# Optimization experiments

Measured on AMD Instinct MI355X. Metric: run time of the kernel, lower is better.

## Reference

```python
import jax, jax.numpy as jnp
import numpy as np

N = 100000      # nodes
E = 1600000     # edges (avg degree 16)
DIN = 128       # input_dim
H = 64          # hidden_dim -> intermediate width 2*H = 128
BN_EPS = 1e-5


def setup_inputs() -> dict:
    key = jax.random.key(0)
    ks = jax.random.split(key, 6)
    x = jax.random.normal(ks[0], (N, DIN), dtype=jnp.float32)
    edge_index = jax.random.randint(ks[1], (2, E), 0, N, dtype=jnp.int64)
    W1 = jax.random.normal(ks[2], (DIN, 2 * H), dtype=jnp.float32) / np.sqrt(DIN).astype(np.float32)
    b1 = jnp.zeros((2 * H,), jnp.float32)
    W2 = jax.random.normal(ks[3], (2 * H, H), dtype=jnp.float32) / np.sqrt(2 * H).astype(np.float32)
    b2 = jnp.zeros((H,), jnp.float32)
    gamma = jnp.ones((2 * H,), jnp.float32)
    beta = jnp.zeros((2 * H,), jnp.float32)
    prelu_a = jnp.asarray(0.25, jnp.float32)  # PReLU default single weight
    return {"x": x, "edge_index": edge_index, "W1": W1, "b1": b1,
            "W2": W2, "b2": b2, "gamma": gamma, "beta": beta, "prelu_a": prelu_a}


def _gcn_conv(x, W, b, src, dst, n):
    # PyG GCNConv (edge_weight=None): lin -> add self-loops -> sym-norm aggregate -> +bias
    h = x @ W                                             # [N, F]
    loops = jnp.arange(n, dtype=src.dtype)
    s = jnp.concatenate([src, loops])                     # [E+N]
    d = jnp.concatenate([dst, loops])
    deg = jax.ops.segment_sum(jnp.ones_like(s, jnp.float32), d, num_segments=n)
    dinv = jnp.where(deg > 0, jax.lax.rsqrt(deg), 0.0)    # deg^{-1/2}, 0 for isolated
    norm = dinv[s] * dinv[d]                              # [E+N]
    out = jax.ops.segment_sum(h[s] * norm[:, None], d, num_segments=n)
    return out + b


def reference(x, edge_index, W1, b1, W2, b2, gamma, beta, prelu_a):
    src, dst = edge_index[0], edge_index[1]
    z = _gcn_conv(x, W1, b1, src, dst, N)                 # conv1: [N, 2H]
    mean = jnp.mean(z, axis=0)                            # BatchNorm1d (training stats)
    var = jnp.var(z, axis=0)
    z = (z - mean) * (gamma * jax.lax.rsqrt(var + BN_EPS)) + beta
    z = jnp.where(z >= 0, z, prelu_a * z)                 # PReLU
    z = _gcn_conv(z, W2, b2, src, dst, N)                 # conv2: [N, H]
    return z
```

## Files before the change

### kernel.cpp

```cpp
#include <hip/hip_runtime.h>


#define DIN 128
#define F1  128
#define F2  64
#define BN_EPS 1e-5f
#define NODE_BSHIFT 8
#define NODE_BMASK  255
#define CHUNK 8192

typedef __attribute__((ext_vector_type(8))) short bf16x8;
typedef __attribute__((ext_vector_type(4))) float f32x4;
typedef __attribute__((ext_vector_type(2))) float f32x2;

__device__ __forceinline__ unsigned short f2bf(float f) {
    unsigned int u = __float_as_uint(f);
    u = u + 0x7fffu + ((u >> 16) & 1u);
    return (unsigned short)(u >> 16);
}
__device__ __forceinline__ float bf2f(unsigned short u) { return __uint_as_float((unsigned int)u << 16); }
__device__ __forceinline__ float bf_lo(unsigned int v) { return __uint_as_float(v << 16); }
__device__ __forceinline__ float bf_hi(unsigned int v) { return __uint_as_float(v & 0xffff0000u); }


__global__ __launch_bounds__(256) void hist_k(const int* __restrict__ dst,
                                              int* __restrict__ bucketcnt,
                                              int e, int nbuck) {
    __shared__ int lh[512];
    int t = threadIdx.x;
    for (int i = t; i < 512; i += 256) lh[i] = 0;
    __syncthreads();
    int base = blockIdx.x * CHUNK;
    int end = base + CHUNK; if (end > e) end = e;
    for (int i = base + t; i < end; i += 256)
        atomicAdd(&lh[dst[i] >> NODE_BSHIFT], 1);
    __syncthreads();
    for (int b = t; b < nbuck; b += 256) {
        int v = lh[b];
        if (v) atomicAdd(&bucketcnt[b], v);
    }
}

__global__ __launch_bounds__(512) void bscan_k(const int* __restrict__ bucketcnt,
                                               int* __restrict__ bucketbase,
                                               int* __restrict__ bucketcur,
                                               int* __restrict__ rowptr,
                                               int nbuck, int n, int e) {
    __shared__ int s[512];
    int t = threadIdx.x;
    int orig = (t < nbuck) ? bucketcnt[t] : 0;
    s[t] = orig;
    __syncthreads();
    int run = orig;
    for (int ofs = 1; ofs < 512; ofs <<= 1) {
        int y = (t >= ofs) ? s[t - ofs] : 0;
        __syncthreads();
        run += y;
        s[t] = run;
        __syncthreads();
    }
    if (t < nbuck) {
        int excl = run - orig;
        bucketbase[t] = excl;
        bucketcur[t] = excl;
    }
    if (t == 0) {
        bucketbase[nbuck] = e;
        rowptr[n] = e;
    }
}

__global__ __launch_bounds__(256) void binpass_k(const int* __restrict__ src,
                                                 const int* __restrict__ dst,
                                                 int* __restrict__ bucketcur,
                                                 int2* __restrict__ pairs, int e) {
    __shared__ int lh[512], lbase[512], lrank[512];
    int t = threadIdx.x;
    for (int i = t; i < 512; i += 256) { lh[i] = 0; lrank[i] = 0; }
    __syncthreads();
    int base = blockIdx.x * CHUNK;
    int end = base + CHUNK; if (end > e) end = e;
    for (int i = base + t; i < end; i += 256)
        atomicAdd(&lh[dst[i] >> NODE_BSHIFT], 1);
    __syncthreads();
    for (int b = t; b < 512; b += 256) {
        int v = lh[b];
        lbase[b] = v ? atomicAdd(&bucketcur[b], v) : 0;
    }
    __syncthreads();
    for (int i = base + t; i < end; i += 256) {
        int sv = src[i], dv = dst[i];
        int b = dv >> NODE_BSHIFT;
        int r = atomicAdd(&lrank[b], 1);
        pairs[lbase[b] + r] = make_int2(sv, dv);
    }
}

__global__ __launch_bounds__(256) void bucket_k(const int2* __restrict__ pairs,
                                                const int* __restrict__ bucketbase,
                                                float* __restrict__ dinv,
                                                int* __restrict__ rowptr,
                                                int* __restrict__ srcsorted, int n) {
    __shared__ int lh[256], loff[256], lrank[256];
    int b = blockIdx.x, t = threadIdx.x;
    int e0 = bucketbase[b], e1 = bucketbase[b + 1];
    lh[t] = 0;
    lrank[t] = 0;
    __syncthreads();
    for (int i = e0 + t; i < e1; i += 256)
        atomicAdd(&lh[pairs[i].y & NODE_BMASK], 1);
    __syncthreads();
    int deg = lh[t];
    int run = deg;
    for (int ofs = 1; ofs < 256; ofs <<= 1) {
        int y = (t >= ofs) ? lh[t - ofs] : 0;
        __syncthreads();
        run += y;
        lh[t] = run;
        __syncthreads();
    }
    loff[t] = run - deg;
    int node = (b << NODE_BSHIFT) + t;
    if (node < n) {
        dinv[node] = rsqrtf((float)(deg + 1));
        rowptr[node] = e0 + (run - deg);
    }
    __syncthreads();
    for (int i = e0 + t; i < e1; i += 256) {
        int2 p = pairs[i];
        int lo = p.y & NODE_BMASK;
        int r = atomicAdd(&lrank[lo], 1);
        srcsorted[e0 + loff[lo] + r] = p.x;
    }
}


__global__ __launch_bounds__(512) void gemm1_k(const float* __restrict__ x,
                                               const float* __restrict__ W,
                                               const float* __restrict__ dinv,
                                               unsigned int* __restrict__ h, int n) {
    __shared__ unsigned short wh[128 * 128];
    __shared__ unsigned short wl[128 * 128];
    int t = threadIdx.x;
    for (int i4 = t; i4 < 128 * 32; i4 += 512) {
        int k = i4 >> 5;
        int c0 = (i4 & 31) * 4;
        float4 v = ((const float4*)W)[i4];
        float vv[4] = {v.x, v.y, v.z, v.w};
#pragma unroll
        for (int j = 0; j < 4; j++) {
            int c = c0 + j;
            unsigned short hi = f2bf(vv[j]);
            unsigned short lo = f2bf(vv[j] - bf2f(hi));
            int addr = c * 128 + ((((k >> 3) ^ (c & 15))) << 3) + (k & 7);
            wh[addr] = hi;
            wl[addr] = lo;
        }
    }
    __syncthreads();

    int w = t >> 6, l = t & 63;
    int lr = l & 15, lg = l >> 4;
    int rowbase = blockIdx.x * 128;
    int arow = rowbase + w * 16 + lr;
    if (arow >= n) arow = n - 1;

    f32x4 acc[8];
#pragma unroll
    for (int nt = 0; nt < 8; nt++) acc[nt] = (f32x4)(0.0f);

#pragma unroll
    for (int ks = 0; ks < 4; ks++) {
        const float4* ap = (const float4*)(x + (size_t)arow * 128 + ks * 32 + lg * 8);
        float4 v0 = ap[0], v1 = ap[1];
        float vv[8] = {v0.x, v0.y, v0.z, v0.w, v1.x, v1.y, v1.z, v1.w};
        bf16x8 ah, al;
#pragma unroll
        for (int j = 0; j < 8; j++) {
            unsigned short hi = f2bf(vv[j]);
            ah[j] = (short)hi;
            al[j] = (short)f2bf(vv[j] - bf2f(hi));
        }
#pragma unroll
        for (int nt = 0; nt < 8; nt++) {
            int ao = (nt * 16 + lr) * 128 + (((4 * ks + lg) ^ lr) << 3);
            bf16x8 bh = *(const bf16x8*)&wh[ao];
            bf16x8 bl = *(const bf16x8*)&wl[ao];
            acc[nt] = __builtin_amdgcn_mfma_f32_16x16x32_bf16(ah, bh, acc[nt], 0, 0, 0);
            acc[nt] = __builtin_amdgcn_mfma_f32_16x16x32_bf16(al, bh, acc[nt], 0, 0, 0);
            acc[nt] = __builtin_amdgcn_mfma_f32_16x16x32_bf16(ah, bl, acc[nt], 0, 0, 0);
        }
    }
    __syncthreads();
    unsigned short* ob = wh;
#pragma unroll
    for (int r = 0; r < 4; r++) {
        int rl = w * 16 + lg * 4 + r;
        int grow = rowbase + rl;
        float di = dinv[grow < n ? grow : 0];
#pragma unroll
        for (int nt = 0; nt < 8; nt++)
            ob[rl * 128 + nt * 16 + lr] = f2bf(acc[nt][r] * di);
    }
    __syncthreads();
    const unsigned int* ob32 = (const unsigned int*)ob;
    for (int i = t; i < 128 * 64; i += 512) {
        int rl = i >> 6, cu = i & 63;
        int grow = rowbase + rl;
        if (grow < n) h[(size_t)grow * 64 + cu] = ob32[rl * 64 + cu];
    }
}


__global__ __launch_bounds__(64) void agg1_k(const unsigned int* __restrict__ h,
                                             const float* __restrict__ dinv,
                                             const int* __restrict__ rowptr,
                                             const int* __restrict__ srcs,
                                             const float* __restrict__ b1,
                                             float* __restrict__ z, int n) {
    int nd = blockIdx.x;
    int f = threadIdx.x;
    float di = dinv[nd];
    unsigned int sv = h[(size_t)nd * 64 + f];
    float ax = bf_lo(sv);
    float ay = bf_hi(sv);
    int e = rowptr[nd], e1 = rowptr[nd + 1];
    for (; e + 8 <= e1; e += 8) {
        int s0 = srcs[e],     s1 = srcs[e + 1], s2 = srcs[e + 2], s3 = srcs[e + 3];
        int s4 = srcs[e + 4], s5 = srcs[e + 5], s6 = srcs[e + 6], s7 = srcs[e + 7];
        unsigned int v0 = h[(size_t)s0 * 64 + f];
        unsigned int v1 = h[(size_t)s1 * 64 + f];
        unsigned int v2 = h[(size_t)s2 * 64 + f];
        unsigned int v3 = h[(size_t)s3 * 64 + f];
        unsigned int v4 = h[(size_t)s4 * 64 + f];
        unsigned int v5 = h[(size_t)s5 * 64 + f];
        unsigned int v6 = h[(size_t)s6 * 64 + f];
        unsigned int v7 = h[(size_t)s7 * 64 + f];
        ax += bf_lo(v0) + bf_lo(v1) + bf_lo(v2) + bf_lo(v3);
        ay += bf_hi(v0) + bf_hi(v1) + bf_hi(v2) + bf_hi(v3);
        ax += bf_lo(v4) + bf_lo(v5) + bf_lo(v6) + bf_lo(v7);
        ay += bf_hi(v4) + bf_hi(v5) + bf_hi(v6) + bf_hi(v7);
    }
    for (; e < e1; e++) {
        unsigned int v = h[(size_t)srcs[e] * 64 + f];
        ax += bf_lo(v);
        ay += bf_hi(v);
    }
    float2 bb = ((const float2*)b1)[f];
    f32x2 o;
    o.x = fmaf(ax, di, bb.x);
    o.y = fmaf(ay, di, bb.y);
    __builtin_nontemporal_store(o, (f32x2*)z + (size_t)nd * 64 + f);
}


__global__ __launch_bounds__(256) void bnstats_k(const float* __restrict__ z,
                                                 double* __restrict__ bnacc, int n) {
    __shared__ float reds[8][128];
    __shared__ float redq[8][128];
    int t = threadIdx.x;
    int q = t >> 5;
    int c = t & 31;
    const float4* z4 = (const float4*)z;
    float4 s = make_float4(0.f, 0.f, 0.f, 0.f);
    float4 sq = make_float4(0.f, 0.f, 0.f, 0.f);
    int stride = gridDim.x * 8;
#pragma unroll 2
    for (int r = blockIdx.x * 8 + q; r < n; r += stride) {
        float4 v = z4[(size_t)r * 32 + c];
        s.x += v.x; s.y += v.y; s.z += v.z; s.w += v.w;
        sq.x = fmaf(v.x, v.x, sq.x);
        sq.y = fmaf(v.y, v.y, sq.y);
        sq.z = fmaf(v.z, v.z, sq.z);
        sq.w = fmaf(v.w, v.w, sq.w);
    }
    *(float4*)&reds[q][c * 4] = s;
    *(float4*)&redq[q][c * 4] = sq;
    __syncthreads();
    if (t < 128) {
        float ssum = 0.f, qsum = 0.f;
#pragma unroll
        for (int i = 0; i < 8; i++) {
            ssum += reds[i][t];
            qsum += redq[i][t];
        }
        int copy = (blockIdx.x & 3) * 256;
        atomicAdd(&bnacc[copy + t], (double)ssum);
        atomicAdd(&bnacc[copy + 128 + t], (double)qsum);
    }
}


__global__ __launch_bounds__(512) void gemm2_k(const float* __restrict__ z,
                                               const float* __restrict__ W,
                                               const double* __restrict__ bnacc,
                                               const float* __restrict__ gamma,
                                               const float* __restrict__ beta,
                                               const float* __restrict__ prelu_a,
                                               const float* __restrict__ dinv,
                                               unsigned int* __restrict__ h2, int n) {
    __shared__ unsigned short wh[64 * 128];
    __shared__ unsigned short wl[64 * 128];
    __shared__ float lsc[128], lsh[128];
    int t = threadIdx.x;
    for (int i4 = t; i4 < 128 * 16; i4 += 512) {
        int k = i4 >> 4;
        int c0 = (i4 & 15) * 4;
        float4 v = ((const float4*)W)[i4];
        float vv[4] = {v.x, v.y, v.z, v.w};
#pragma unroll
        for (int j = 0; j < 4; j++) {
            int c = c0 + j;
            unsigned short hi = f2bf(vv[j]);
            unsigned short lo = f2bf(vv[j] - bf2f(hi));
            int addr = c * 128 + ((((k >> 3) ^ (c & 15))) << 3) + (k & 7);
            wh[addr] = hi;
            wl[addr] = lo;
        }
    }
    if (t < 128) {
        double sm = 0.0, qq = 0.0;
#pragma unroll
        for (int cpy = 0; cpy < 4; cpy++) {
            sm += bnacc[cpy * 256 + t];
            qq += bnacc[cpy * 256 + 128 + t];
        }
        double mean = sm / n;
        double var = qq / n - mean * mean;
        float sc = gamma[t] * rsqrtf((float)var + BN_EPS);
        lsc[t] = sc;
        lsh[t] = beta[t] - (float)mean * sc;
    }
    __syncthreads();

    float pa = prelu_a[0];
    int w = t >> 6, l = t & 63;
    int lr = l & 15, lg = l >> 4;
    int rowbase = blockIdx.x * 128;
    int arow = rowbase + w * 16 + lr;
    if (arow >= n) arow = n - 1;

    f32x4 acc[4];
#pragma unroll
    for (int nt = 0; nt < 4; nt++) acc[nt] = (f32x4)(0.0f);

#pragma unroll
    for (int ks = 0; ks < 4; ks++) {
        const float4* ap = (const float4*)(z + (size_t)arow * 128 + ks * 32 + lg * 8);
        float4 v0 = ap[0], v1 = ap[1];
        const float4* sc4 = (const float4*)&lsc[ks * 32 + lg * 8];
        const float4* sh4 = (const float4*)&lsh[ks * 32 + lg * 8];
        float4 s0 = sc4[0], s1 = sc4[1];
        float4 t0 = sh4[0], t1 = sh4[1];
        float vv[8];
        vv[0] = fmaf(v0.x, s0.x, t0.x); vv[1] = fmaf(v0.y, s0.y, t0.y);
        vv[2] = fmaf(v0.z, s0.z, t0.z); vv[3] = fmaf(v0.w, s0.w, t0.w);
        vv[4] = fmaf(v1.x, s1.x, t1.x); vv[5] = fmaf(v1.y, s1.y, t1.y);
        vv[6] = fmaf(v1.z, s1.z, t1.z); vv[7] = fmaf(v1.w, s1.w, t1.w);
        bf16x8 ah, al;
#pragma unroll
        for (int j = 0; j < 8; j++) {
            float y = vv[j] >= 0.f ? vv[j] : pa * vv[j];
            unsigned short hi = f2bf(y);
            ah[j] = (short)hi;
            al[j] = (short)f2bf(y - bf2f(hi));
        }
#pragma unroll
        for (int nt = 0; nt < 4; nt++) {
            int ao = (nt * 16 + lr) * 128 + (((4 * ks + lg) ^ lr) << 3);
            bf16x8 bh = *(const bf16x8*)&wh[ao];
            bf16x8 bl = *(const bf16x8*)&wl[ao];
            acc[nt] = __builtin_amdgcn_mfma_f32_16x16x32_bf16(ah, bh, acc[nt], 0, 0, 0);
            acc[nt] = __builtin_amdgcn_mfma_f32_16x16x32_bf16(al, bh, acc[nt], 0, 0, 0);
            acc[nt] = __builtin_amdgcn_mfma_f32_16x16x32_bf16(ah, bl, acc[nt], 0, 0, 0);
        }
    }
    __syncthreads();
    unsigned short* ob = wh;
#pragma unroll
    for (int r = 0; r < 4; r++) {
        int rl = w * 16 + lg * 4 + r;
        int grow = rowbase + rl;
        float di = dinv[grow < n ? grow : 0];
#pragma unroll
        for (int nt = 0; nt < 4; nt++)
            ob[rl * 64 + nt * 16 + lr] = f2bf(acc[nt][r] * di);
    }
    __syncthreads();
    const unsigned int* ob32 = (const unsigned int*)ob;
    for (int i = t; i < 128 * 32; i += 512) {
        int rl = i >> 5, cu = i & 31;
        int grow = rowbase + rl;
        if (grow < n) h2[(size_t)grow * 32 + cu] = ob32[rl * 32 + cu];
    }
}


__global__ __launch_bounds__(64) void agg2_k(const unsigned short* __restrict__ hs,
                                             const float* __restrict__ dinv,
                                             const int* __restrict__ rowptr,
                                             const int* __restrict__ srcs,
                                             const float* __restrict__ b2,
                                             float* __restrict__ out, int n) {
    int nd = blockIdx.x;
    int f = threadIdx.x;
    float di = dinv[nd];
    float acc = bf2f(hs[(size_t)nd * F2 + f]);
    int e = rowptr[nd], e1 = rowptr[nd + 1];
    for (; e + 8 <= e1; e += 8) {
        int s0 = srcs[e],     s1 = srcs[e + 1], s2 = srcs[e + 2], s3 = srcs[e + 3];
        int s4 = srcs[e + 4], s5 = srcs[e + 5], s6 = srcs[e + 6], s7 = srcs[e + 7];
        float h0 = bf2f(hs[(size_t)s0 * F2 + f]);
        float h1 = bf2f(hs[(size_t)s1 * F2 + f]);
        float h2 = bf2f(hs[(size_t)s2 * F2 + f]);
        float h3 = bf2f(hs[(size_t)s3 * F2 + f]);
        float h4 = bf2f(hs[(size_t)s4 * F2 + f]);
        float h5 = bf2f(hs[(size_t)s5 * F2 + f]);
        float h6 = bf2f(hs[(size_t)s6 * F2 + f]);
        float h7 = bf2f(hs[(size_t)s7 * F2 + f]);
        acc += h0 + h1 + h2 + h3;
        acc += h4 + h5 + h6 + h7;
    }
    for (; e < e1; e++)
        acc += bf2f(hs[(size_t)srcs[e] * F2 + f]);
    float o = fmaf(acc, di, b2[f]);
    __builtin_nontemporal_store(o, out + (size_t)nd * F2 + f);
}


extern "C" void kernel_launch(void* const* d_in, const int* in_sizes, int n_in,
                              void* d_out, int out_size, void* d_ws, size_t ws_size,
                              hipStream_t stream) {
    const float* x       = (const float*)d_in[0];
    const int*   ei      = (const int*)d_in[1];
    const float* W1      = (const float*)d_in[2];
    const float* b1      = (const float*)d_in[3];
    const float* W2      = (const float*)d_in[4];
    const float* b2      = (const float*)d_in[5];
    const float* gamma   = (const float*)d_in[6];
    const float* beta    = (const float*)d_in[7];
    const float* prelu_a = (const float*)d_in[8];

    const int N = in_sizes[0] / DIN;
    const int E = in_sizes[1] / 2;
    const int* src = ei;
    const int* dst = ei + E;
    const int NBUCK = (N + NODE_BMASK) >> NODE_BSHIFT;

    char* p = (char*)d_ws;
    size_t off = 0;
    auto take = [&](size_t bytes) -> char* {
        char* r = p + off;
        off = (off + bytes + 255) & ~(size_t)255;
        return r;
    };
    int*            bucketcnt  = (int*)take(512 * 4);
    int*            bucketbase = (int*)take(513 * 4);
    int*            bucketcur  = (int*)take(512 * 4);
    float*          dinv       = (float*)take((size_t)N * 4);
    int*            rowptr     = (int*)take((size_t)(N + 1) * 4);
    int*            srcsorted  = (int*)take((size_t)E * 4);
    int2*           pairs      = (int2*)take((size_t)E * 8);
    double*         bnacc      = (double*)take(4 * 256 * 8);
    unsigned int*   h          = (unsigned int*)take((size_t)N * 64 * 4);
    float*          z          = (float*)take((size_t)N * F1 * 4);
    unsigned int*   h2         = h;
    float*          out        = (float*)d_out;

    hipMemsetAsync(bucketcnt, 0, 512 * 4, stream);
    hipMemsetAsync(bnacc, 0, 4 * 256 * 8, stream);

    const int eb = (E + CHUNK - 1) / CHUNK;

    hist_k<<<eb, 256, 0, stream>>>(dst, bucketcnt, E, NBUCK);
    bscan_k<<<1, 512, 0, stream>>>(bucketcnt, bucketbase, bucketcur, rowptr, NBUCK, N, E);
    binpass_k<<<eb, 256, 0, stream>>>(src, dst, bucketcur, pairs, E);
    bucket_k<<<NBUCK, 256, 0, stream>>>(pairs, bucketbase, dinv, rowptr, srcsorted, N);

    gemm1_k<<<(N + 127) / 128, 512, 0, stream>>>(x, W1, dinv, h, N);
    agg1_k<<<N, 64, 0, stream>>>(h, dinv, rowptr, srcsorted, b1, z, N);
    bnstats_k<<<1024, 256, 0, stream>>>(z, bnacc, N);
    gemm2_k<<<(N + 127) / 128, 512, 0, stream>>>(z, W2, bnacc, gamma, beta, prelu_a, dinv, h2, N);
    agg2_k<<<N, F2, 0, stream>>>((const unsigned short*)h2, dinv, rowptr, srcsorted, b2, out, N);
}
```

Measured before the change: 352.9 us.

## Pre-split weights once and use half-wave wider gathers in aggregation kernels

Adds a small prep kernel that splits W1/W2 into swizzled bf16 hi/lo tables once, so each GEMM block copies them into LDS with 16-byte vector loads instead of recomputing the split per block. Both aggregation kernels now split the 64-lane wave into two halves that each process alternate neighbours with wider per-lane loads (8 or 4 bytes), then combine via a cross-half shuffle. This fetches each neighbour row with fewer, larger loads and doubles gather parallelism per node. The cost is an extra kernel launch, extra workspace, and half the lanes idle during the final store.

```diff
diff --git a/kernel.cpp b/kernel.cpp
--- a/kernel.cpp
+++ b/kernel.cpp
@@ -10,6 +10,7 @@
 #define CHUNK 8192
 
 typedef __attribute__((ext_vector_type(8))) short bf16x8;
+typedef __attribute__((ext_vector_type(8))) unsigned short u16x8;
 typedef __attribute__((ext_vector_type(4))) float f32x4;
 typedef __attribute__((ext_vector_type(2))) float f32x2;
 
@@ -135,27 +136,58 @@
 }
 
 
+__global__ __launch_bounds__(256) void wprep_k(const float* __restrict__ W1,
+                                               const float* __restrict__ W2,
+                                               unsigned short* __restrict__ wt1h,
+                                               unsigned short* __restrict__ wt1l,
+                                               unsigned short* __restrict__ wt2h,
+                                               unsigned short* __restrict__ wt2l) {
+    int t = blockIdx.x * 256 + threadIdx.x;
+    if (t < 2048) {
+        int c = t >> 4, k8 = (t & 15) * 8;
+        u16x8 hv, lv;
+#pragma unroll
+        for (int j = 0; j < 8; j++) {
+            float v = W1[(size_t)(k8 + j) * 128 + c];
+            unsigned short hi = f2bf(v);
+            hv[j] = hi;
+            lv[j] = f2bf(v - bf2f(hi));
+        }
+        int addr = c * 128 + (((k8 >> 3) ^ (c & 15)) << 3);
+        *(u16x8*)&wt1h[addr] = hv;
+        *(u16x8*)&wt1l[addr] = lv;
+    } else if (t < 3072) {
+        int tt = t - 2048;
+        int c = tt >> 4, k8 = (tt & 15) * 8;
+        u16x8 hv, lv;
+#pragma unroll
+        for (int j = 0; j < 8; j++) {
+            float v = W2[(size_t)(k8 + j) * 64 + c];
+            unsigned short hi = f2bf(v);
+            hv[j] = hi;
+            lv[j] = f2bf(v - bf2f(hi));
+        }
+        int addr = c * 128 + (((k8 >> 3) ^ (c & 15)) << 3);
+        *(u16x8*)&wt2h[addr] = hv;
+        *(u16x8*)&wt2l[addr] = lv;
+    }
+}
+
+
 __global__ __launch_bounds__(512) void gemm1_k(const float* __restrict__ x,
-                                               const float* __restrict__ W,
+                                               const unsigned short* __restrict__ wt1h,
+                                               const unsigned short* __restrict__ wt1l,
                                                const float* __restrict__ dinv,
                                                unsigned int* __restrict__ h, int n) {
     __shared__ unsigned short wh[128 * 128];
     __shared__ unsigned short wl[128 * 128];
     int t = threadIdx.x;
-    for (int i4 = t; i4 < 128 * 32; i4 += 512) {
-        int k = i4 >> 5;
-        int c0 = (i4 & 31) * 4;
-        float4 v = ((const float4*)W)[i4];
-        float vv[4] = {v.x, v.y, v.z, v.w};
-#pragma unroll
-        for (int j = 0; j < 4; j++) {
-            int c = c0 + j;
-            unsigned short hi = f2bf(vv[j]);
-            unsigned short lo = f2bf(vv[j] - bf2f(hi));
-            int addr = c * 128 + ((((k >> 3) ^ (c & 15))) << 3) + (k & 7);
-            wh[addr] = hi;
-            wl[addr] = lo;
-        }
+    {
+        const uint4* gh = (const uint4*)wt1h;
+        const uint4* gl = (const uint4*)wt1l;
+        uint4* dh = (uint4*)wh;
+        uint4* dl = (uint4*)wl;
+        for (int i = t; i < 2048; i += 512) { dh[i] = gh[i]; dl[i] = gl[i]; }
     }
     __syncthreads();
 
@@ -219,38 +251,72 @@
                                              const float* __restrict__ b1,
                                              float* __restrict__ z, int n) {
     int nd = blockIdx.x;
-    int f = threadIdx.x;
+    int l = threadIdx.x;
+    int half = l >> 5;
+    int q = l & 31;
+    const uint2* hrow = (const uint2*)h;
     float di = dinv[nd];
-    unsigned int sv = h[(size_t)nd * 64 + f];
-    float ax = bf_lo(sv);
-    float ay = bf_hi(sv);
-    int e = rowptr[nd], e1 = rowptr[nd + 1];
-    for (; e + 8 <= e1; e += 8) {
-        int s0 = srcs[e],     s1 = srcs[e + 1], s2 = srcs[e + 2], s3 = srcs[e + 3];
-        int s4 = srcs[e + 4], s5 = srcs[e + 5], s6 = srcs[e + 6], s7 = srcs[e + 7];
-        unsigned int v0 = h[(size_t)s0 * 64 + f];
-        unsigned int v1 = h[(size_t)s1 * 64 + f];
-        unsigned int v2 = h[(size_t)s2 * 64 + f];
-        unsigned int v3 = h[(size_t)s3 * 64 + f];
-        unsigned int v4 = h[(size_t)s4 * 64 + f];
-        unsigned int v5 = h[(size_t)s5 * 64 + f];
-        unsigned int v6 = h[(size_t)s6 * 64 + f];
-        unsigned int v7 = h[(size_t)s7 * 64 + f];
-        ax += bf_lo(v0) + bf_lo(v1) + bf_lo(v2) + bf_lo(v3);
-        ay += bf_hi(v0) + bf_hi(v1) + bf_hi(v2) + bf_hi(v3);
-        ax += bf_lo(v4) + bf_lo(v5) + bf_lo(v6) + bf_lo(v7);
-        ay += bf_hi(v4) + bf_hi(v5) + bf_hi(v6) + bf_hi(v7);
-    }
-    for (; e < e1; e++) {
-        unsigned int v = h[(size_t)srcs[e] * 64 + f];
-        ax += bf_lo(v);
-        ay += bf_hi(v);
-    }
-    float2 bb = ((const float2*)b1)[f];
-    f32x2 o;
-    o.x = fmaf(ax, di, bb.x);
-    o.y = fmaf(ay, di, bb.y);
-    __builtin_nontemporal_store(o, (f32x2*)z + (size_t)nd * 64 + f);
+    float a0 = 0.f, a1 = 0.f, a2 = 0.f, a3 = 0.f;
+    int e0 = rowptr[nd];
+    int cnt = rowptr[nd + 1] - e0 + 1;
+    int v = half;
+    if (v < cnt) {
+        int s = (v == 0) ? nd : srcs[e0 + v - 1];
+        uint2 u = hrow[(size_t)s * 32 + q];
+        a0 += bf_lo(u.x); a1 += bf_hi(u.x); a2 += bf_lo(u.y); a3 += bf_hi(u.y);
+    }
+    v += 2;
+    for (; v + 14 < cnt; v += 16) {
+        int i0 = e0 + v - 1;
+        int s0 = srcs[i0],      s1 = srcs[i0 + 2],  s2 = srcs[i0 + 4],  s3 = srcs[i0 + 6];
+        int s4 = srcs[i0 + 8],  s5 = srcs[i0 + 10], s6 = srcs[i0 + 12], s7 = srcs[i0 + 14];
+        uint2 u0 = hrow[(size_t)s0 * 32 + q];
+        uint2 u1 = hrow[(size_t)s1 * 32 + q];
+        uint2 u2 = hrow[(size_t)s2 * 32 + q];
+        uint2 u3 = hrow[(size_t)s3 * 32 + q];
+        uint2 u4 = hrow[(size_t)s4 * 32 + q];
+        uint2 u5 = hrow[(size_t)s5 * 32 + q];
+        uint2 u6 = hrow[(size_t)s6 * 32 + q];
+        uint2 u7 = hrow[(size_t)s7 * 32 + q];
+        a0 += bf_lo(u0.x) + bf_lo(u1.x) + bf_lo(u2.x) + bf_lo(u3.x);
+        a1 += bf_hi(u0.x) + bf_hi(u1.x) + bf_hi(u2.x) + bf_hi(u3.x);
+        a2 += bf_lo(u0.y) + bf_lo(u1.y) + bf_lo(u2.y) + bf_lo(u3.y);
+        a3 += bf_hi(u0.y) + bf_hi(u1.y) + bf_hi(u2.y) + bf_hi(u3.y);
+        a0 += bf_lo(u4.x) + bf_lo(u5.x) + bf_lo(u6.x) + bf_lo(u7.x);
+        a1 += bf_hi(u4.x) + bf_hi(u5.x) + bf_hi(u6.x) + bf_hi(u7.x);
+        a2 += bf_lo(u4.y) + bf_lo(u5.y) + bf_lo(u6.y) + bf_lo(u7.y);
+        a3 += bf_hi(u4.y) + bf_hi(u5.y) + bf_hi(u6.y) + bf_hi(u7.y);
+    }
+    for (; v + 6 < cnt; v += 8) {
+        int i0 = e0 + v - 1;
+        int s0 = srcs[i0], s1 = srcs[i0 + 2], s2 = srcs[i0 + 4], s3 = srcs[i0 + 6];
+        uint2 u0 = hrow[(size_t)s0 * 32 + q];
+        uint2 u1 = hrow[(size_t)s1 * 32 + q];
+        uint2 u2 = hrow[(size_t)s2 * 32 + q];
+        uint2 u3 = hrow[(size_t)s3 * 32 + q];
+        a0 += bf_lo(u0.x) + bf_lo(u1.x) + bf_lo(u2.x) + bf_lo(u3.x);
+        a1 += bf_hi(u0.x) + bf_hi(u1.x) + bf_hi(u2.x) + bf_hi(u3.x);
+        a2 += bf_lo(u0.y) + bf_lo(u1.y) + bf_lo(u2.y) + bf_lo(u3.y);
+        a3 += bf_hi(u0.y) + bf_hi(u1.y) + bf_hi(u2.y) + bf_hi(u3.y);
+    }
+    for (; v < cnt; v += 2) {
+        int s = srcs[e0 + v - 1];
+        uint2 u = hrow[(size_t)s * 32 + q];
+        a0 += bf_lo(u.x); a1 += bf_hi(u.x); a2 += bf_lo(u.y); a3 += bf_hi(u.y);
+    }
+    a0 += __shfl_xor(a0, 32);
+    a1 += __shfl_xor(a1, 32);
+    a2 += __shfl_xor(a2, 32);
+    a3 += __shfl_xor(a3, 32);
+    if (half == 0) {
+        float4 bb = ((const float4*)b1)[q];
+        f32x4 o;
+        o.x = fmaf(a0, di, bb.x);
+        o.y = fmaf(a1, di, bb.y);
+        o.z = fmaf(a2, di, bb.z);
+        o.w = fmaf(a3, di, bb.w);
+        __builtin_nontemporal_store(o, (f32x4*)z + (size_t)nd * 32 + q);
+    }
 }
 
 
@@ -292,7 +358,8 @@
 
 
 __global__ __launch_bounds__(512) void gemm2_k(const float* __restrict__ z,
-                                               const float* __restrict__ W,
+                                               const unsigned short* __restrict__ wt2h,
+                                               const unsigned short* __restrict__ wt2l,
                                                const double* __restrict__ bnacc,
                                                const float* __restrict__ gamma,
                                                const float* __restrict__ beta,
@@ -303,20 +370,12 @@
     __shared__ unsigned short wl[64 * 128];
     __shared__ float lsc[128], lsh[128];
     int t = threadIdx.x;
-    for (int i4 = t; i4 < 128 * 16; i4 += 512) {
-        int k = i4 >> 4;
-        int c0 = (i4 & 15) * 4;
-        float4 v = ((const float4*)W)[i4];
-        float vv[4] = {v.x, v.y, v.z, v.w};
-#pragma unroll
-        for (int j = 0; j < 4; j++) {
-            int c = c0 + j;
-            unsigned short hi = f2bf(vv[j]);
-            unsigned short lo = f2bf(vv[j] - bf2f(hi));
-            int addr = c * 128 + ((((k >> 3) ^ (c & 15))) << 3) + (k & 7);
-            wh[addr] = hi;
-            wl[addr] = lo;
-        }
+    {
+        const uint4* gh = (const uint4*)wt2h;
+        const uint4* gl = (const uint4*)wt2l;
+        uint4* dh = (uint4*)wh;
+        uint4* dl = (uint4*)wl;
+        for (int i = t; i < 1024; i += 512) { dh[i] = gh[i]; dl[i] = gl[i]; }
     }
     if (t < 128) {
         double sm = 0.0, qq = 0.0;
@@ -396,35 +455,68 @@
 }
 
 
-__global__ __launch_bounds__(64) void agg2_k(const unsigned short* __restrict__ hs,
+__global__ __launch_bounds__(64) void agg2_k(const unsigned int* __restrict__ hs,
                                              const float* __restrict__ dinv,
                                              const int* __restrict__ rowptr,
                                              const int* __restrict__ srcs,
                                              const float* __restrict__ b2,
                                              float* __restrict__ out, int n) {
     int nd = blockIdx.x;
-    int f = threadIdx.x;
+    int l = threadIdx.x;
+    int half = l >> 5;
+    int q = l & 31;
     float di = dinv[nd];
-    float acc = bf2f(hs[(size_t)nd * F2 + f]);
-    int e = rowptr[nd], e1 = rowptr[nd + 1];
-    for (; e + 8 <= e1; e += 8) {
-        int s0 = srcs[e],     s1 = srcs[e + 1], s2 = srcs[e + 2], s3 = srcs[e + 3];
-        int s4 = srcs[e + 4], s5 = srcs[e + 5], s6 = srcs[e + 6], s7 = srcs[e + 7];
-        float h0 = bf2f(hs[(size_t)s0 * F2 + f]);
-        float h1 = bf2f(hs[(size_t)s1 * F2 + f]);
-        float h2 = bf2f(hs[(size_t)s2 * F2 + f]);
-        float h3 = bf2f(hs[(size_t)s3 * F2 + f]);
-        float h4 = bf2f(hs[(size_t)s4 * F2 + f]);
-        float h5 = bf2f(hs[(size_t)s5 * F2 + f]);
-        float h6 = bf2f(hs[(size_t)s6 * F2 + f]);
-        float h7 = bf2f(hs[(size_t)s7 * F2 + f]);
-        acc += h0 + h1 + h2 + h3;
-        acc += h4 + h5 + h6 + h7;
-    }
-    for (; e < e1; e++)
-        acc += bf2f(hs[(size_t)srcs[e] * F2 + f]);
-    float o = fmaf(acc, di, b2[f]);
-    __builtin_nontemporal_store(o, out + (size_t)nd * F2 + f);
+    float a0 = 0.f, a1 = 0.f;
+    int e0 = rowptr[nd];
+    int cnt = rowptr[nd + 1] - e0 + 1;
+    int v = half;
+    if (v < cnt) {
+        int s = (v == 0) ? nd : srcs[e0 + v - 1];
+        unsigned int u = hs[(size_t)s * 32 + q];
+        a0 += bf_lo(u); a1 += bf_hi(u);
+    }
+    v += 2;
+    for (; v + 14 < cnt; v += 16) {
+        int i0 = e0 + v - 1;
+        int s0 = srcs[i0],      s1 = srcs[i0 + 2],  s2 = srcs[i0 + 4],  s3 = srcs[i0 + 6];
+        int s4 = srcs[i0 + 8],  s5 = srcs[i0 + 10], s6 = srcs[i0 + 12], s7 = srcs[i0 + 14];
+        unsigned int u0 = hs[(size_t)s0 * 32 + q];
+        unsigned int u1 = hs[(size_t)s1 * 32 + q];
+        unsigned int u2 = hs[(size_t)s2 * 32 + q];
+        unsigned int u3 = hs[(size_t)s3 * 32 + q];
+        unsigned int u4 = hs[(size_t)s4 * 32 + q];
+        unsigned int u5 = hs[(size_t)s5 * 32 + q];
+        unsigned int u6 = hs[(size_t)s6 * 32 + q];
+        unsigned int u7 = hs[(size_t)s7 * 32 + q];
+        a0 += bf_lo(u0) + bf_lo(u1) + bf_lo(u2) + bf_lo(u3);
+        a1 += bf_hi(u0) + bf_hi(u1) + bf_hi(u2) + bf_hi(u3);
+        a0 += bf_lo(u4) + bf_lo(u5) + bf_lo(u6) + bf_lo(u7);
+        a1 += bf_hi(u4) + bf_hi(u5) + bf_hi(u6) + bf_hi(u7);
+    }
+    for (; v + 6 < cnt; v += 8) {
+        int i0 = e0 + v - 1;
+        int s0 = srcs[i0], s1 = srcs[i0 + 2], s2 = srcs[i0 + 4], s3 = srcs[i0 + 6];
+        unsigned int u0 = hs[(size_t)s0 * 32 + q];
+        unsigned int u1 = hs[(size_t)s1 * 32 + q];
+        unsigned int u2 = hs[(size_t)s2 * 32 + q];
+        unsigned int u3 = hs[(size_t)s3 * 32 + q];
+        a0 += bf_lo(u0) + bf_lo(u1) + bf_lo(u2) + bf_lo(u3);
+        a1 += bf_hi(u0) + bf_hi(u1) + bf_hi(u2) + bf_hi(u3);
+    }
+    for (; v < cnt; v += 2) {
+        int s = srcs[e0 + v - 1];
+        unsigned int u = hs[(size_t)s * 32 + q];
+        a0 += bf_lo(u); a1 += bf_hi(u);
+    }
+    a0 += __shfl_xor(a0, 32);
+    a1 += __shfl_xor(a1, 32);
+    if (half == 0) {
+        float2 bb = ((const float2*)b2)[q];
+        f32x2 o;
+        o.x = fmaf(a0, di, bb.x);
+        o.y = fmaf(a1, di, bb.y);
+        __builtin_nontemporal_store(o, (f32x2*)out + (size_t)nd * 32 + q);
+    }
 }
 
 
@@ -462,6 +554,10 @@
     int*            srcsorted  = (int*)take((size_t)E * 4);
     int2*           pairs      = (int2*)take((size_t)E * 8);
     double*         bnacc      = (double*)take(4 * 256 * 8);
+    unsigned short* wt1h       = (unsigned short*)take(128 * 128 * 2);
+    unsigned short* wt1l       = (unsigned short*)take(128 * 128 * 2);
+    unsigned short* wt2h       = (unsigned short*)take(64 * 128 * 2);
+    unsigned short* wt2l       = (unsigned short*)take(64 * 128 * 2);
     unsigned int*   h          = (unsigned int*)take((size_t)N * 64 * 4);
     float*          z          = (float*)take((size_t)N * F1 * 4);
     unsigned int*   h2         = h;
@@ -472,14 +568,15 @@
 
     const int eb = (E + CHUNK - 1) / CHUNK;
 
+    wprep_k<<<12, 256, 0, stream>>>(W1, W2, wt1h, wt1l, wt2h, wt2l);
     hist_k<<<eb, 256, 0, stream>>>(dst, bucketcnt, E, NBUCK);
     bscan_k<<<1, 512, 0, stream>>>(bucketcnt, bucketbase, bucketcur, rowptr, NBUCK, N, E);
     binpass_k<<<eb, 256, 0, stream>>>(src, dst, bucketcur, pairs, E);
     bucket_k<<<NBUCK, 256, 0, stream>>>(pairs, bucketbase, dinv, rowptr, srcsorted, N);
 
-    gemm1_k<<<(N + 127) / 128, 512, 0, stream>>>(x, W1, dinv, h, N);
+    gemm1_k<<<(N + 127) / 128, 512, 0, stream>>>(x, wt1h, wt1l, dinv, h, N);
     agg1_k<<<N, 64, 0, stream>>>(h, dinv, rowptr, srcsorted, b1, z, N);
     bnstats_k<<<1024, 256, 0, stream>>>(z, bnacc, N);
-    gemm2_k<<<(N + 127) / 128, 512, 0, stream>>>(z, W2, bnacc, gamma, beta, prelu_a, dinv, h2, N);
-    agg2_k<<<N, F2, 0, stream>>>((const unsigned short*)h2, dinv, rowptr, srcsorted, b2, out, N);
-}
+    gemm2_k<<<(N + 127) / 128, 512, 0, stream>>>(z, wt2h, wt2l, bnacc, gamma, beta, prelu_a, dinv, h2, N);
+    agg2_k<<<N, F2, 0, stream>>>((const unsigned int*)h2, dinv, rowptr, srcsorted, b2, out, N);
+}
```

After: 342.4 us. -3.0%, faster.
